# Kernel optimization log

Hardware: AMD Instinct MI355X
Metric: run time of the kernel (lower is better)

Reference implementation:

```python
import jax, jax.numpy as jnp
import numpy as np

NUM_HEADS = 16
NEG_INF = float('-inf')


def setup_inputs() -> dict:
    key = jax.random.key(0)
    ks = jax.random.split(key, 8)
    B, S, D = 2, 2048, 1024
    return {
        "query": jax.random.normal(ks[0], (B, S, D), jnp.float32),
        "key": jax.random.normal(ks[1], (B, S, D), jnp.float32),
        "value": jax.random.normal(ks[2], (B, S, D), jnp.float32),
        "attention_mask": jnp.zeros((B, S, S), dtype=bool),
        "Wq": jax.random.normal(ks[3], (D, D), jnp.float32) * (D ** -0.5),
        "Wk": jax.random.normal(ks[4], (D, D), jnp.float32) * (D ** -0.5),
        "Wv": jax.random.normal(ks[5], (D, D), jnp.float32) * (D ** -0.5),
        "Wout": jax.random.normal(ks[6], (D, D), jnp.float32) * (D ** -0.5),
        "b_out": jnp.zeros((D,), jnp.float32),
        "is_causal": 1,
    }


def reference(query, key, value, attention_mask, Wq, Wk, Wv, Wout, b_out, is_causal):
    B, q_len, D = query.shape
    k_len = key.shape[1]
    H = NUM_HEADS
    dk = D // H
    # projections (torch Linear: x @ W.T), split heads -> [B, H, S, dk]
    q = (query @ Wq.T).reshape(B, q_len, H, dk).transpose(0, 2, 1, 3)
    k = (key @ Wk.T).reshape(B, k_len, H, dk).transpose(0, 2, 1, 3)
    v = (value @ Wv.T).reshape(B, k_len, H, dk).transpose(0, 2, 1, 3)
    scores = jnp.einsum('bhqd,bhkd->bhqk', q, k) / jnp.sqrt(jnp.float32(dk))
    if is_causal:
        causal = jnp.triu(jnp.ones((q_len, k_len), dtype=bool), k=1)
        scores = jnp.where(causal, NEG_INF, scores)
    # attn_mask True -> masked out; broadcast over heads
    scores = jnp.where(attention_mask[:, None, :, :], NEG_INF, scores)
    attn = jax.nn.softmax(scores, axis=-1)
    attn = jnp.where(jnp.isnan(attn), 0.0, attn)  # fully-masked rows -> 0
    out = jnp.einsum('bhqk,bhkd->bhqd', attn, v)
    out = out.transpose(0, 2, 1, 3).reshape(B, q_len, D)
    return out @ Wout.T + b_out
```

## Files before the change

kernel.cpp:

```cpp
#include <hip/hip_runtime.h>
#include <hip/hip_bf16.h>

typedef __attribute__((ext_vector_type(8))) short bf16x8;
typedef __attribute__((ext_vector_type(4))) float f32x4;
typedef unsigned long long u64;
typedef unsigned int u32;

#define MFMA(a,b,c) __builtin_amdgcn_mfma_f32_16x16x32_bf16(a,b,c,0,0,0)
#define NEG_INF (-__builtin_inff())
#define SCALE2 0.1803368801111244f

__device__ __forceinline__ unsigned short f2b(float f) {
  unsigned int u = __float_as_uint(f);
  u = u + 0x7fffu + ((u >> 16) & 1u);
  return (unsigned short)(u >> 16);
}

__device__ __forceinline__ u32 pkbf(float lo, float hi) {
  __hip_bfloat162 h = __float22bfloat162_rn(float2{lo, hi});
  return *reinterpret_cast<u32*>(&h);
}

__device__ __forceinline__ void gload_lds16(const unsigned short* g, unsigned short* l) {
  __builtin_amdgcn_global_load_lds((const __attribute__((address_space(1))) void*)g,
                                   (__attribute__((address_space(3))) void*)l, 16, 0, 0);
}

__global__ void cvt7(const float* s0, const float* s1, const float* s2,
                     const float* s3, const float* s4, const float* s5, const float* s6,
                     unsigned short* d0, unsigned short* d1, unsigned short* d2,
                     unsigned short* d3, unsigned short* d4, unsigned short* d5, unsigned short* d6,
                     int nbig, int nsmall) {
  const float* s; unsigned short* d; int n4;
  switch (blockIdx.y) {
    case 0: s=s0; d=d0; n4=nbig; break;
    case 1: s=s1; d=d1; n4=nbig; break;
    case 2: s=s2; d=d2; n4=nbig; break;
    case 3: s=s3; d=d3; n4=nsmall; break;
    case 4: s=s4; d=d4; n4=nsmall; break;
    case 5: s=s5; d=d5; n4=nsmall; break;
    default: s=s6; d=d6; n4=nsmall; break;
  }
  int i = blockIdx.x * blockDim.x + threadIdx.x;
  if (i < n4) {
    float4 v = reinterpret_cast<const float4*>(s)[i];
    ushort4 o;
    o.x = f2b(v.x); o.y = f2b(v.y); o.z = f2b(v.z); o.w = f2b(v.w);
    reinterpret_cast<ushort4*>(d)[i] = o;
  }
}

__global__ void pack_mask(const unsigned char* __restrict__ am, u64* __restrict__ pm, int nU) {
  int lane = threadIdx.x & 63;
  int wid = blockIdx.x * (blockDim.x >> 6) + (threadIdx.x >> 6);
  int stride = gridDim.x * (blockDim.x >> 6);
  for (int u = wid; u < nU; u += stride) {
    unsigned char v = am[(size_t)u * 64 + lane];
    u64 m = __ballot(v != 0);
    if (lane == 0) pm[u] = m;
  }
}

__global__ void mask_summary(const u64* __restrict__ pm, u32* __restrict__ ms, int rows, int nkt) {
  int lane = threadIdx.x & 63;
  int wid = (blockIdx.x * blockDim.x + threadIdx.x) >> 6;
  int nw = (gridDim.x * blockDim.x) >> 6;
  for (int rp = wid; rp < (rows >> 1); rp += nw) {
    int row = rp * 2 + (lane >> 5);
    int t = lane & 31;
    u64 v = pm[(size_t)row * nkt + t];
    u64 bm = __ballot(v != 0ULL);
    if (lane == 0)  ms[rp*2]     = (u32)bm;
    if (lane == 32) ms[rp*2 + 1] = (u32)(bm >> 32);
  }
}

__global__ __launch_bounds__(256) void qkv128s(
    const unsigned short* __restrict__ A,
    const unsigned short* __restrict__ Bw,
    unsigned short* __restrict__ Cqk,
    unsigned short* __restrict__ Cv)
{
  const int K = 1024;
  __shared__ unsigned short As[128*32];
  __shared__ unsigned short Bs[128*32];
  const int tid  = threadIdx.x;
  const int w    = tid >> 6, lane = tid & 63;
  const int wr   = w >> 1,   wc   = w & 1;
  const int g    = lane >> 4, li  = lane & 15;
  const int m0   = blockIdx.x * 128, n0 = blockIdx.y * 128;
  const int bq0  = (m0 >> 12) * 1024 + n0;

  f32x4 acc[4][4] = {};

  const int rS0 = (w*2+0)*16 + (lane>>2);
  const int rS1 = (w*2+1)*16 + (lane>>2);
  const int cS  = (lane&3)*8;
  const unsigned short* gA0 = A  + (size_t)(m0+rS0)*K + cS;
  const unsigned short* gA1 = A  + (size_t)(m0+rS1)*K + cS;
  const unsigned short* gB0 = Bw + (size_t)(bq0+rS0)*K + cS;
  const unsigned short* gB1 = Bw + (size_t)(bq0+rS1)*K + cS;
  unsigned short* lA0 = &As[(w*2+0)*512];
  unsigned short* lA1 = &As[(w*2+1)*512];
  unsigned short* lB0 = &Bs[(w*2+0)*512];
  unsigned short* lB1 = &Bs[(w*2+1)*512];

  for (int k0 = 0; k0 < K; k0 += 32) {
    gload_lds16(gA0 + k0, lA0);
    gload_lds16(gA1 + k0, lA1);
    gload_lds16(gB0 + k0, lB0);
    gload_lds16(gB1 + k0, lB1);
    __syncthreads();

    bf16x8 af[4], bf[4];
    #pragma unroll
    for (int i = 0; i < 4; ++i)
      af[i] = *(const bf16x8*)(&As[(wr*64 + i*16 + li)*32 + g*8]);
    #pragma unroll
    for (int j = 0; j < 4; ++j)
      bf[j] = *(const bf16x8*)(&Bs[(wc*64 + j*16 + li)*32 + g*8]);
    #pragma unroll
    for (int i = 0; i < 4; ++i)
      #pragma unroll
      for (int j = 0; j < 4; ++j)
        acc[i][j] = MFMA(af[i], bf[j], acc[i][j]);
    __syncthreads();
  }

  #pragma unroll
  for (int i = 0; i < 4; ++i) {
    #pragma unroll
    for (int j = 0; j < 4; ++j) {
      int col = n0 + wc*64 + j*16 + li;
      #pragma unroll
      for (int r = 0; r < 4; ++r) {
        int row = m0 + wr*64 + i*16 + g*4 + r;
        float v = acc[i][j][r];
        if (row < 8192) {
          size_t addr = (((size_t)(row >> 11) * 16 + (col >> 6)) * 2048 + (row & 2047)) * 64 + (col & 63);
          Cqk[addr] = f2b(v);
        } else {
          int tk = row & 4095;
          size_t addr = (((size_t)(tk >> 11) * 16 + (col >> 6)) * 64 + (col & 63)) * 2048 + (tk & 2047);
          Cv[addr] = f2b(v);
        }
      }
    }
  }
}

__global__ __launch_bounds__(256) void gemm64x64(
    const unsigned short* __restrict__ A,
    const unsigned short* __restrict__ Bw,
    float* __restrict__ Cf,
    const float* __restrict__ bias,
    int M, int N, int K)
{
  const int NT = 32;
  __shared__ unsigned short As[2][64*32];
  __shared__ unsigned short Bs[2][64*32];
  const int tid  = threadIdx.x;
  const int w    = tid >> 6, lane = tid & 63;
  const int wr   = w >> 1,   wc   = w & 1;
  const int g    = lane >> 4, li  = lane & 15;
  const int m0   = blockIdx.x * 64, n0 = blockIdx.y * 64;

  f32x4 acc[2][2] = {};
  const int crow = lane >> 2, ccol = (lane & 3) * 8;
  const unsigned short* gA = A  + (size_t)(m0 + w*16 + crow)*K + ccol;
  const unsigned short* gB = Bw + (size_t)(n0 + w*16 + crow)*K + ccol;

  gload_lds16(gA, &As[0][w*512]);
  gload_lds16(gB, &Bs[0][w*512]);
  __syncthreads();

  for (int t = 0; t < NT; ++t) {
    const int cur = t & 1;
    if (t + 1 < NT) {
      const int k1 = (t + 1) * 32;
      gload_lds16(gA + k1, &As[cur^1][w*512]);
      gload_lds16(gB + k1, &Bs[cur^1][w*512]);
    }
    bf16x8 af[2], bf[2];
    #pragma unroll
    for (int i = 0; i < 2; ++i)
      af[i] = *(const bf16x8*)(&As[cur][(wr*32 + i*16 + li)*32 + g*8]);
    #pragma unroll
    for (int j = 0; j < 2; ++j)
      bf[j] = *(const bf16x8*)(&Bs[cur][(wc*32 + j*16 + li)*32 + g*8]);
    #pragma unroll
    for (int i = 0; i < 2; ++i)
      #pragma unroll
      for (int j = 0; j < 2; ++j)
        acc[i][j] = MFMA(af[i], bf[j], acc[i][j]);
    __syncthreads();
  }

  #pragma unroll
  for (int i = 0; i < 2; ++i) {
    #pragma unroll
    for (int j = 0; j < 2; ++j) {
      int col = n0 + wc*32 + j*16 + li;
      #pragma unroll
      for (int r = 0; r < 4; ++r) {
        int row = m0 + wr*32 + i*16 + g*4 + r;
        Cf[(size_t)row*N + col] = acc[i][j][r] + bias[col];
      }
    }
  }
}

__global__ __launch_bounds__(256, 4) void attn_kernel(
    const unsigned short* __restrict__ Qh,
    const unsigned short* __restrict__ Kh,
    const unsigned short* __restrict__ Vt,
    const u64* __restrict__ pmask,
    const u32* __restrict__ msum,
    const int* __restrict__ causal_p,
    unsigned short* __restrict__ Ob,
    int B, int H, int S)
{
  __shared__ unsigned short Ks [64*64];
  __shared__ unsigned short Vts[64*64];

  const int tid = threadIdx.x, w = tid >> 6, lane = tid & 63;
  const int g = lane >> 4, li = lane & 15;
  const int nkt = S >> 6, nqt = S >> 6;
  const int causal = causal_p[0];

  int id = blockIdx.x;
  int par = (id ^ (id >> 8)) & 1;
  int qh  = ((id >> 1) & 15) ^ (((id >> 8) & 3) << 2);
  int bh  = id >> 5;
  int qt  = par ? (nqt - 1 - qh) : qh;
  const int q0 = qt << 6;
  const int b = bh / H, h = bh % H;
  const size_t baseK = (size_t)bh * S * 64;
  const size_t baseV = (size_t)bh * 64 * S;

  const int qg = q0 + w*16 + li;
  const unsigned short* qp = Qh + baseK + (size_t)qg*64 + g*8;
  const bf16x8 qf0 = *(const bf16x8*)(qp);
  const bf16x8 qf1 = *(const bf16x8*)(qp + 32);

  const u32 sOr = msum[(size_t)b*S + qg];

  f32x4 oacc[4] = {};
  float mrun = -1e30f, lrun = 0.f;

  const int colk  = (lane & 7) ^ ((lane >> 3) & 7);
  const int ldrow = lane >> 3;
  const int ntile = causal ? (qt + 1) : nkt;

  for (int t = 0; t < ntile; ++t) {
    const int kv0 = t << 6;
    __syncthreads();
    #pragma unroll
    for (int s2 = 0; s2 < 2; ++s2) {
      int u = w*2 + s2;
      gload_lds16(Kh + baseK + (size_t)(kv0 + u*8 + ldrow)*64 + colk*8, &Ks[u*512]);
      gload_lds16(Vt + baseV + (size_t)(u*8 + ldrow)*S + kv0 + colk*8, &Vts[u*512]);
    }
    __syncthreads();

    f32x4 sa[4];
    #pragma unroll
    for (int ni = 0; ni < 4; ++ni) sa[ni] = (f32x4){0.f, 0.f, 0.f, 0.f};
    #pragma unroll
    for (int ni = 0; ni < 4; ++ni) {
      int row = ni*16 + li, rx = row & 7;
      bf16x8 k0 = *(const bf16x8*)(&Ks[row*64 + ((g     ^ rx))*8]);
      bf16x8 k1 = *(const bf16x8*)(&Ks[row*64 + (((4+g) ^ rx))*8]);
      sa[ni] = MFMA(k0, qf0, sa[ni]);
      sa[ni] = MFMA(k1, qf1, sa[ni]);
    }

    const bool edge   = (causal != 0) && (t == ntile - 1);
    const bool doMask = __any(((sOr >> t) & 1u) != 0u);
    float corr = 1.0f;
    bool rescale = true;

    if (!edge && !doMask) {
      float pe[4][4];
      #pragma unroll
      for (int ni = 0; ni < 4; ++ni)
        #pragma unroll
        for (int r = 0; r < 4; ++r)
          pe[ni][r] = exp2f(fmaf(sa[ni][r], SCALE2, -mrun));
      float a0 = fmaxf(sa[0][0], sa[0][1]), a1 = fmaxf(sa[0][2], sa[0][3]);
      float a2 = fmaxf(sa[1][0], sa[1][1]), a3 = fmaxf(sa[1][2], sa[1][3]);
      float a4 = fmaxf(sa[2][0], sa[2][1]), a5 = fmaxf(sa[2][2], sa[2][3]);
      float a6 = fmaxf(sa[3][0], sa[3][1]), a7 = fmaxf(sa[3][2], sa[3][3]);
      float mx = fmaxf(fmaxf(fmaxf(a0,a1), fmaxf(a2,a3)),
                       fmaxf(fmaxf(a4,a5), fmaxf(a6,a7)));
      mx = fmaxf(mx, __shfl_xor(mx, 16));
      mx = fmaxf(mx, __shfl_xor(mx, 32));
      float mxs = mx * SCALE2;
      if (__all(mxs <= mrun + 8.0f)) {
        float s0 = (pe[0][0]+pe[0][1]) + (pe[0][2]+pe[0][3]);
        float s1 = (pe[1][0]+pe[1][1]) + (pe[1][2]+pe[1][3]);
        float s2 = (pe[2][0]+pe[2][1]) + (pe[2][2]+pe[2][3]);
        float s3 = (pe[3][0]+pe[3][1]) + (pe[3][2]+pe[3][3]);
        float rs = (s0+s1) + (s2+s3);
        rs += __shfl_xor(rs, 16);
        rs += __shfl_xor(rs, 32);
        lrun += rs;
        #pragma unroll
        for (int ni = 0; ni < 4; ++ni)
          #pragma unroll
          for (int r = 0; r < 4; ++r)
            sa[ni][r] = pe[ni][r];
        rescale = false;
      } else {
        float mu = fmaxf(mrun, mxs);
        corr = exp2f(mrun - mu);
        float rs = 0.f;
        #pragma unroll
        for (int ni = 0; ni < 4; ++ni)
          #pragma unroll
          for (int r = 0; r < 4; ++r) {
            float p = exp2f(fmaf(sa[ni][r], SCALE2, -mu));
            sa[ni][r] = p;
            rs += p;
          }
        rs += __shfl_xor(rs, 16);
        rs += __shfl_xor(rs, 32);
        lrun = lrun * corr + rs;
        mrun = mu;
      }
    } else {
      u64 mrow = doMask ? pmask[((size_t)b*S + qg) * nkt + t] : 0ULL;
      #pragma unroll
      for (int ni = 0; ni < 4; ++ni)
        #pragma unroll
        for (int r = 0; r < 4; ++r) {
          int kvloc = ni*16 + g*4 + r;
          bool dead = (edge && (kv0 + kvloc > qg)) || ((mrow >> kvloc) & 1ULL);
          sa[ni][r] = dead ? NEG_INF : sa[ni][r] * SCALE2;
        }
      float mx = sa[0][0];
      #pragma unroll
      for (int ni = 0; ni < 4; ++ni)
        #pragma unroll
        for (int r = 0; r < 4; ++r)
          if (ni + r) mx = fmaxf(mx, sa[ni][r]);
      mx = fmaxf(mx, __shfl_xor(mx, 16));
      mx = fmaxf(mx, __shfl_xor(mx, 32));
      float mu = fmaxf(mrun, mx);
      corr = exp2f(mrun - mu);
      float rs = 0.f;
      #pragma unroll
      for (int ni = 0; ni < 4; ++ni)
        #pragma unroll
        for (int r = 0; r < 4; ++r) {
          float pe = exp2f(sa[ni][r] - mu);
          sa[ni][r] = pe;
          rs += pe;
        }
      rs += __shfl_xor(rs, 16);
      rs += __shfl_xor(rs, 32);
      lrun = lrun * corr + rs;
      mrun = mu;
    }

    bf16x8 pf[2];
    #pragma unroll
    for (int c = 0; c < 2; ++c) {
      u32 PA0 = pkbf(sa[2*c  ][0], sa[2*c  ][1]);
      u32 PA1 = pkbf(sa[2*c  ][2], sa[2*c  ][3]);
      u32 PB0 = pkbf(sa[2*c+1][0], sa[2*c+1][1]);
      u32 PB1 = pkbf(sa[2*c+1][2], sa[2*c+1][3]);
      u32 X16_0 = (u32)__shfl_xor((int)((g==2) ? PB0 : PA0), 16);
      u32 X16_1 = (u32)__shfl_xor((int)((g==2) ? PB1 : PA1), 16);
      u32 X32_0 = (u32)__shfl_xor((int)((g==0) ? PB0 : PA0), 32);
      u32 X32_1 = (u32)__shfl_xor((int)((g==0) ? PB1 : PA1), 32);
      u32 X48_0 = (u32)__shfl_xor((int)((g==1) ? PB0 : PA0), 48);
      u32 X48_1 = (u32)__shfl_xor((int)((g==1) ? PB1 : PA1), 48);
      union { u32 u[4]; bf16x8 v; } pbu;
      pbu.u[0] = (g==0) ? PA0   : (g==1) ? X48_0 : (g==2) ? X32_0 : X16_0;
      pbu.u[1] = (g==0) ? PA1   : (g==1) ? X48_1 : (g==2) ? X32_1 : X16_1;
      pbu.u[2] = (g==0) ? X16_0 : (g==1) ? X32_0 : (g==2) ? X48_0 : PB0;
      pbu.u[3] = (g==0) ? X16_1 : (g==1) ? X32_1 : (g==2) ? X48_1 : PB1;
      pf[c] = pbu.v;
    }

    if (rescale) {
      #pragma unroll
      for (int di = 0; di < 4; ++di) {
        oacc[di][0] *= corr; oacc[di][1] *= corr;
        oacc[di][2] *= corr; oacc[di][3] *= corr;
      }
    }

    #pragma unroll
    for (int c = 0; c < 2; ++c) {
      #pragma unroll
      for (int di = 0; di < 4; ++di) {
        int d = di*16 + li;
        bf16x8 vf = *(const bf16x8*)(&Vts[d*64 + (((c*4+g) ^ (d&7)))*8]);
        oacc[di] = MFMA(vf, pf[c], oacc[di]);
      }
    }
  }

  __syncthreads();
  unsigned short* scr = &Ks[w*1024];
  float rl = (lrun > 0.f) ? 1.0f / lrun : 0.f;
  #pragma unroll
  for (int di = 0; di < 4; ++di)
    #pragma unroll
    for (int r = 0; r < 4; ++r) {
      int d = di*16 + g*4 + r;
      scr[li*64 + (((d>>3) ^ (li&7)))*8 + (d&7)] = f2b(oacc[di][r] * rl);
    }
  const int D = H * 64;
  #pragma unroll
  for (int rr = 0; rr < 2; ++rr) {
    int q = rr*8 + (lane >> 3);
    int sl = lane & 7;
    bf16x8 v = *(const bf16x8*)(&scr[q*64 + ((sl ^ (q & 7)))*8]);
    *(bf16x8*)(Ob + (size_t)(b*S + q0 + w*16 + q)*D + h*64 + sl*8) = v;
  }
}

extern "C" void kernel_launch(void* const* d_in, const int* in_sizes, int n_in,
                              void* d_out, int out_size, void* d_ws, size_t ws_size,
                              hipStream_t stream) {
  const float* query = (const float*)d_in[0];
  const float* key_  = (const float*)d_in[1];
  const float* value = (const float*)d_in[2];
  const unsigned char* amask = (const unsigned char*)d_in[3];
  const float* Wq   = (const float*)d_in[4];
  const float* Wk   = (const float*)d_in[5];
  const float* Wv   = (const float*)d_in[6];
  const float* Wout = (const float*)d_in[7];
  const float* b_out = (const float*)d_in[8];
  const int* is_causal = (const int*)d_in[9];
  float* out = (float*)d_out;

  const int B = 2, S = 2048, D = 1024, H = 16;
  const int M = B * S;
  const size_t nx = (size_t)M * D;
  const size_t nw = (size_t)D * D;
  const int nU = B * S * (S / 64);

  unsigned short* ws = (unsigned short*)d_ws;
  unsigned short* xq = ws;
  unsigned short* xk = xq + nx;
  unsigned short* xv = xk + nx;
  unsigned short* wq = xv + nx;
  unsigned short* wk = wq + nw;
  unsigned short* wv = wk + nw;
  unsigned short* wo = wv + nw;
  unsigned short* qb = wo + nw;
  unsigned short* kb = qb + nx;
  unsigned short* vt = kb + nx;
  u32* msum = (u32*)(vt + nx);
  unsigned short* ob = xq;
  u64* pmask = (u64*)xv;

  cvt7<<<dim3((unsigned)(nx/4/256), 7), 256, 0, stream>>>(
      query, key_, value, Wq, Wk, Wv, Wout,
      xq, xk, xv, wq, wk, wv, wo, (int)(nx/4), (int)(nw/4));

  qkv128s<<<dim3(3*M/128, D/128), 256, 0, stream>>>(xq, wq, qb, vt);

  pack_mask<<<512, 256, 0, stream>>>(amask, pmask, nU);
  mask_summary<<<128, 256, 0, stream>>>(pmask, msum, M, S/64);

  attn_kernel<<<dim3((S/64) * B * H), 256, 0, stream>>>(qb, kb, vt, pmask, msum, is_causal, ob, B, H, S);

  gemm64x64<<<dim3(M/64, D/64), 256, 0, stream>>>(ob, wo, out, b_out, M, D, D);
}
```

Before: 168.0 us.

## Split causal attention KV range across blocks with split-K combine kernel

Replaces the one-block-per-query-tile attention grid with a split-KV scheme. Longer causal query tiles are split into 2-4 segments so per-block work is more even, and the grid grows to 2560 blocks. Partial outputs (bf16), row maxima and sums go to workspace, and a new combine kernel merges them with log-sum-exp weights. This targets tail imbalance from the causal triangle. The cost is an extra launch, extra global traffic for the partials, and bf16 rounding of the unnormalized partial outputs.

```diff
diff --git a/kernel.cpp b/kernel.cpp
--- a/kernel.cpp
+++ b/kernel.cpp
@@ -14,6 +14,11 @@
   unsigned int u = __float_as_uint(f);
   u = u + 0x7fffu + ((u >> 16) & 1u);
   return (unsigned short)(u >> 16);
+}
+
+__device__ __forceinline__ float b2f(unsigned short s) {
+  unsigned int u = ((unsigned int)s) << 16;
+  return __uint_as_float(u);
 }
 
 __device__ __forceinline__ u32 pkbf(float lo, float hi) {
@@ -210,6 +215,151 @@
   }
 }
 
+__device__ __forceinline__ void attn_tile(
+    const unsigned short* __restrict__ Ks, const unsigned short* __restrict__ Vts,
+    const bf16x8& qf0, const bf16x8& qf1,
+    float& mrun, float& lrun, f32x4* oacc,
+    bool edge, bool doMask, const u64* __restrict__ prow,
+    int t, int kv0, int qg, int g, int li)
+{
+  f32x4 sa[4];
+  #pragma unroll
+  for (int ni = 0; ni < 4; ++ni) sa[ni] = (f32x4){0.f, 0.f, 0.f, 0.f};
+  #pragma unroll
+  for (int ni = 0; ni < 4; ++ni) {
+    int row = ni*16 + li, rx = row & 7;
+    bf16x8 k0 = *(const bf16x8*)(&Ks[row*64 + ((g     ^ rx))*8]);
+    bf16x8 k1 = *(const bf16x8*)(&Ks[row*64 + (((4+g) ^ rx))*8]);
+    sa[ni] = MFMA(k0, qf0, sa[ni]);
+    sa[ni] = MFMA(k1, qf1, sa[ni]);
+  }
+
+  float corr = 1.0f;
+  bool rescale = true;
+
+  if (!edge && !doMask) {
+    float pe[4][4];
+    #pragma unroll
+    for (int ni = 0; ni < 4; ++ni)
+      #pragma unroll
+      for (int r = 0; r < 4; ++r)
+        pe[ni][r] = exp2f(fmaf(sa[ni][r], SCALE2, -mrun));
+    float a0 = fmaxf(sa[0][0], sa[0][1]), a1 = fmaxf(sa[0][2], sa[0][3]);
+    float a2 = fmaxf(sa[1][0], sa[1][1]), a3 = fmaxf(sa[1][2], sa[1][3]);
+    float a4 = fmaxf(sa[2][0], sa[2][1]), a5 = fmaxf(sa[2][2], sa[2][3]);
+    float a6 = fmaxf(sa[3][0], sa[3][1]), a7 = fmaxf(sa[3][2], sa[3][3]);
+    float mx = fmaxf(fmaxf(fmaxf(a0,a1), fmaxf(a2,a3)),
+                     fmaxf(fmaxf(a4,a5), fmaxf(a6,a7)));
+    mx = fmaxf(mx, __shfl_xor(mx, 16));
+    mx = fmaxf(mx, __shfl_xor(mx, 32));
+    float mxs = mx * SCALE2;
+    if (__all(mxs <= mrun + 8.0f)) {
+      float s0 = (pe[0][0]+pe[0][1]) + (pe[0][2]+pe[0][3]);
+      float s1 = (pe[1][0]+pe[1][1]) + (pe[1][2]+pe[1][3]);
+      float s2 = (pe[2][0]+pe[2][1]) + (pe[2][2]+pe[2][3]);
+      float s3 = (pe[3][0]+pe[3][1]) + (pe[3][2]+pe[3][3]);
+      float rs = (s0+s1) + (s2+s3);
+      rs += __shfl_xor(rs, 16);
+      rs += __shfl_xor(rs, 32);
+      lrun += rs;
+      #pragma unroll
+      for (int ni = 0; ni < 4; ++ni)
+        #pragma unroll
+        for (int r = 0; r < 4; ++r)
+          sa[ni][r] = pe[ni][r];
+      rescale = false;
+    } else {
+      float mu = fmaxf(mrun, mxs);
+      corr = exp2f(mrun - mu);
+      float rs = 0.f;
+      #pragma unroll
+      for (int ni = 0; ni < 4; ++ni)
+        #pragma unroll
+        for (int r = 0; r < 4; ++r) {
+          float p = exp2f(fmaf(sa[ni][r], SCALE2, -mu));
+          sa[ni][r] = p;
+          rs += p;
+        }
+      rs += __shfl_xor(rs, 16);
+      rs += __shfl_xor(rs, 32);
+      lrun = lrun * corr + rs;
+      mrun = mu;
+    }
+  } else {
+    u64 mrow = doMask ? prow[t] : 0ULL;
+    #pragma unroll
+    for (int ni = 0; ni < 4; ++ni)
+      #pragma unroll
+      for (int r = 0; r < 4; ++r) {
+        int kvloc = ni*16 + g*4 + r;
+        bool dead = (edge && (kv0 + kvloc > qg)) || ((mrow >> kvloc) & 1ULL);
+        sa[ni][r] = dead ? NEG_INF : sa[ni][r] * SCALE2;
+      }
+    float mx = sa[0][0];
+    #pragma unroll
+    for (int ni = 0; ni < 4; ++ni)
+      #pragma unroll
+      for (int r = 0; r < 4; ++r)
+        if (ni + r) mx = fmaxf(mx, sa[ni][r]);
+    mx = fmaxf(mx, __shfl_xor(mx, 16));
+    mx = fmaxf(mx, __shfl_xor(mx, 32));
+    float mu = fmaxf(mrun, mx);
+    corr = exp2f(mrun - mu);
+    float rs = 0.f;
+    #pragma unroll
+    for (int ni = 0; ni < 4; ++ni)
+      #pragma unroll
+      for (int r = 0; r < 4; ++r) {
+        float pe = exp2f(sa[ni][r] - mu);
+        sa[ni][r] = pe;
+        rs += pe;
+      }
+    rs += __shfl_xor(rs, 16);
+    rs += __shfl_xor(rs, 32);
+    lrun = lrun * corr + rs;
+    mrun = mu;
+  }
+
+  bf16x8 pf[2];
+  #pragma unroll
+  for (int c = 0; c < 2; ++c) {
+    u32 PA0 = pkbf(sa[2*c  ][0], sa[2*c  ][1]);
+    u32 PA1 = pkbf(sa[2*c  ][2], sa[2*c  ][3]);
+    u32 PB0 = pkbf(sa[2*c+1][0], sa[2*c+1][1]);
+    u32 PB1 = pkbf(sa[2*c+1][2], sa[2*c+1][3]);
+    u32 X16_0 = (u32)__shfl_xor((int)((g==2) ? PB0 : PA0), 16);
+    u32 X16_1 = (u32)__shfl_xor((int)((g==2) ? PB1 : PA1), 16);
+    u32 X32_0 = (u32)__shfl_xor((int)((g==0) ? PB0 : PA0), 32);
+    u32 X32_1 = (u32)__shfl_xor((int)((g==0) ? PB1 : PA1), 32);
+    u32 X48_0 = (u32)__shfl_xor((int)((g==1) ? PB0 : PA0), 48);
+    u32 X48_1 = (u32)__shfl_xor((int)((g==1) ? PB1 : PA1), 48);
+    union { u32 u[4]; bf16x8 v; } pbu;
+    pbu.u[0] = (g==0) ? PA0   : (g==1) ? X48_0 : (g==2) ? X32_0 : X16_0;
+    pbu.u[1] = (g==0) ? PA1   : (g==1) ? X48_1 : (g==2) ? X32_1 : X16_1;
+    pbu.u[2] = (g==0) ? X16_0 : (g==1) ? X32_0 : (g==2) ? X48_0 : PB0;
+    pbu.u[3] = (g==0) ? X16_1 : (g==1) ? X32_1 : (g==2) ? X48_1 : PB1;
+    pf[c] = pbu.v;
+  }
+
+  if (rescale) {
+    #pragma unroll
+    for (int di = 0; di < 4; ++di) {
+      oacc[di][0] *= corr; oacc[di][1] *= corr;
+      oacc[di][2] *= corr; oacc[di][3] *= corr;
+    }
+  }
+
+  #pragma unroll
+  for (int c = 0; c < 2; ++c) {
+    #pragma unroll
+    for (int di = 0; di < 4; ++di) {
+      int d = di*16 + li;
+      bf16x8 vf = *(const bf16x8*)(&Vts[d*64 + (((c*4+g) ^ (d&7)))*8]);
+      oacc[di] = MFMA(vf, pf[c], oacc[di]);
+    }
+  }
+}
+
 __global__ __launch_bounds__(256, 4) void attn_kernel(
     const unsigned short* __restrict__ Qh,
     const unsigned short* __restrict__ Kh,
@@ -218,6 +368,9 @@
     const u32* __restrict__ msum,
     const int* __restrict__ causal_p,
     unsigned short* __restrict__ Ob,
+    unsigned short* __restrict__ Opart,
+    float* __restrict__ Mp,
+    float* __restrict__ Lp,
     int B, int H, int S)
 {
   __shared__ unsigned short Ks [64*64];
@@ -225,34 +378,47 @@
 
   const int tid = threadIdx.x, w = tid >> 6, lane = tid & 63;
   const int g = lane >> 4, li = lane & 15;
-  const int nkt = S >> 6, nqt = S >> 6;
+  const int nkt = S >> 6;
   const int causal = causal_p[0];
-
-  int id = blockIdx.x;
-  int par = (id ^ (id >> 8)) & 1;
-  int qh  = ((id >> 1) & 15) ^ (((id >> 8) & 3) << 2);
-  int bh  = id >> 5;
-  int qt  = par ? (nqt - 1 - qh) : qh;
-  const int q0 = qt << 6;
-  const int b = bh / H, h = bh % H;
+  const int j = blockIdx.x;
+
+  int bh, qt, seg, k, t0, t1;
+  if (causal) {
+    bh = j / 80;
+    int jj = 79 - (j - bh*80);
+    if (jj < 8)       { qt = jj;              seg = 0;      k = 1; }
+    else if (jj < 24) { int x = jj-8;  qt = 8  + (x>>1); seg = x&1;      k = 2; }
+    else if (jj < 48) { int x = jj-24; int q3 = x/3; qt = 16 + q3; seg = x - q3*3; k = 3; }
+    else              { int x = jj-48; qt = 24 + (x>>2); seg = x&3;      k = 4; }
+    int nt = qt + 1;
+    t0 = (seg*nt)/k; t1 = ((seg+1)*nt)/k;
+  } else {
+    if (j >= 2048) return;
+    bh = j >> 6;
+    int jj = j & 63;
+    qt = jj >> 1; seg = jj & 1; k = 2;
+    t0 = seg*16; t1 = t0 + 16;
+  }
+
+  const int b = bh >> 4, h = bh & 15;
   const size_t baseK = (size_t)bh * S * 64;
   const size_t baseV = (size_t)bh * 64 * S;
-
+  const int colk  = (lane & 7) ^ ((lane >> 3) & 7);
+  const int ldrow = lane >> 3;
+  const int D = H * 64;
+
+  const int q0 = qt << 6;
   const int qg = q0 + w*16 + li;
   const unsigned short* qp = Qh + baseK + (size_t)qg*64 + g*8;
   const bf16x8 qf0 = *(const bf16x8*)(qp);
   const bf16x8 qf1 = *(const bf16x8*)(qp + 32);
-
   const u32 sOr = msum[(size_t)b*S + qg];
+  const u64* prow = pmask + (size_t)(b*S + qg) * nkt;
 
   f32x4 oacc[4] = {};
   float mrun = -1e30f, lrun = 0.f;
 
-  const int colk  = (lane & 7) ^ ((lane >> 3) & 7);
-  const int ldrow = lane >> 3;
-  const int ntile = causal ? (qt + 1) : nkt;
-
-  for (int t = 0; t < ntile; ++t) {
+  for (int t = t0; t < t1; ++t) {
     const int kv0 = t << 6;
     __syncthreads();
     #pragma unroll
@@ -262,165 +428,107 @@
       gload_lds16(Vt + baseV + (size_t)(u*8 + ldrow)*S + kv0 + colk*8, &Vts[u*512]);
     }
     __syncthreads();
-
-    f32x4 sa[4];
-    #pragma unroll
-    for (int ni = 0; ni < 4; ++ni) sa[ni] = (f32x4){0.f, 0.f, 0.f, 0.f};
-    #pragma unroll
-    for (int ni = 0; ni < 4; ++ni) {
-      int row = ni*16 + li, rx = row & 7;
-      bf16x8 k0 = *(const bf16x8*)(&Ks[row*64 + ((g     ^ rx))*8]);
-      bf16x8 k1 = *(const bf16x8*)(&Ks[row*64 + (((4+g) ^ rx))*8]);
-      sa[ni] = MFMA(k0, qf0, sa[ni]);
-      sa[ni] = MFMA(k1, qf1, sa[ni]);
-    }
-
-    const bool edge   = (causal != 0) && (t == ntile - 1);
+    const bool edge = (causal != 0) && (t == qt);
     const bool doMask = __any(((sOr >> t) & 1u) != 0u);
-    float corr = 1.0f;
-    bool rescale = true;
-
-    if (!edge && !doMask) {
-      float pe[4][4];
-      #pragma unroll
-      for (int ni = 0; ni < 4; ++ni)
-        #pragma unroll
-        for (int r = 0; r < 4; ++r)
-          pe[ni][r] = exp2f(fmaf(sa[ni][r], SCALE2, -mrun));
-      float a0 = fmaxf(sa[0][0], sa[0][1]), a1 = fmaxf(sa[0][2], sa[0][3]);
-      float a2 = fmaxf(sa[1][0], sa[1][1]), a3 = fmaxf(sa[1][2], sa[1][3]);
-      float a4 = fmaxf(sa[2][0], sa[2][1]), a5 = fmaxf(sa[2][2], sa[2][3]);
-      float a6 = fmaxf(sa[3][0], sa[3][1]), a7 = fmaxf(sa[3][2], sa[3][3]);
-      float mx = fmaxf(fmaxf(fmaxf(a0,a1), fmaxf(a2,a3)),
-                       fmaxf(fmaxf(a4,a5), fmaxf(a6,a7)));
-      mx = fmaxf(mx, __shfl_xor(mx, 16));
-      mx = fmaxf(mx, __shfl_xor(mx, 32));
-      float mxs = mx * SCALE2;
-      if (__all(mxs <= mrun + 8.0f)) {
-        float s0 = (pe[0][0]+pe[0][1]) + (pe[0][2]+pe[0][3]);
-        float s1 = (pe[1][0]+pe[1][1]) + (pe[1][2]+pe[1][3]);
-        float s2 = (pe[2][0]+pe[2][1]) + (pe[2][2]+pe[2][3]);
-        float s3 = (pe[3][0]+pe[3][1]) + (pe[3][2]+pe[3][3]);
-        float rs = (s0+s1) + (s2+s3);
-        rs += __shfl_xor(rs, 16);
-        rs += __shfl_xor(rs, 32);
-        lrun += rs;
-        #pragma unroll
-        for (int ni = 0; ni < 4; ++ni)
-          #pragma unroll
-          for (int r = 0; r < 4; ++r)
-            sa[ni][r] = pe[ni][r];
-        rescale = false;
-      } else {
-        float mu = fmaxf(mrun, mxs);
-        corr = exp2f(mrun - mu);
-        float rs = 0.f;
-        #pragma unroll
-        for (int ni = 0; ni < 4; ++ni)
-          #pragma unroll
-          for (int r = 0; r < 4; ++r) {
-            float p = exp2f(fmaf(sa[ni][r], SCALE2, -mu));
-            sa[ni][r] = p;
-            rs += p;
-          }
-        rs += __shfl_xor(rs, 16);
-        rs += __shfl_xor(rs, 32);
-        lrun = lrun * corr + rs;
-        mrun = mu;
+    attn_tile(Ks, Vts, qf0, qf1, mrun, lrun, oacc, edge, doMask, prow, t, kv0, qg, g, li);
+  }
+
+  if (k == 1) {
+    __syncthreads();
+    unsigned short* scr = &Ks[w*1024];
+    float rl = (lrun > 0.f) ? 1.0f / lrun : 0.f;
+    #pragma unroll
+    for (int di = 0; di < 4; ++di)
+      #pragma unroll
+      for (int r = 0; r < 4; ++r) {
+        int d = di*16 + g*4 + r;
+        scr[li*64 + (((d>>3) ^ (li&7)))*8 + (d&7)] = f2b(oacc[di][r] * rl);
       }
+    #pragma unroll
+    for (int rr = 0; rr < 2; ++rr) {
+      int q = rr*8 + (lane >> 3);
+      int sl = lane & 7;
+      bf16x8 v = *(const bf16x8*)(&scr[q*64 + ((sl ^ (q & 7)))*8]);
+      *(bf16x8*)(Ob + (size_t)(b*S + q0 + w*16 + q)*D + h*64 + sl*8) = v;
+    }
+  } else {
+    int local;
+    if (causal) {
+      local = (qt < 16) ? (2*(qt-8) + seg)
+            : (qt < 24) ? (16 + 3*(qt-16) + seg)
+                        : (40 + 4*(qt-24) + seg);
     } else {
-      u64 mrow = doMask ? pmask[((size_t)b*S + qg) * nkt + t] : 0ULL;
-      #pragma unroll
-      for (int ni = 0; ni < 4; ++ni)
-        #pragma unroll
-        for (int r = 0; r < 4; ++r) {
-          int kvloc = ni*16 + g*4 + r;
-          bool dead = (edge && (kv0 + kvloc > qg)) || ((mrow >> kvloc) & 1ULL);
-          sa[ni][r] = dead ? NEG_INF : sa[ni][r] * SCALE2;
-        }
-      float mx = sa[0][0];
-      #pragma unroll
-      for (int ni = 0; ni < 4; ++ni)
-        #pragma unroll
-        for (int r = 0; r < 4; ++r)
-          if (ni + r) mx = fmaxf(mx, sa[ni][r]);
-      mx = fmaxf(mx, __shfl_xor(mx, 16));
-      mx = fmaxf(mx, __shfl_xor(mx, 32));
-      float mu = fmaxf(mrun, mx);
-      corr = exp2f(mrun - mu);
-      float rs = 0.f;
-      #pragma unroll
-      for (int ni = 0; ni < 4; ++ni)
-        #pragma unroll
-        for (int r = 0; r < 4; ++r) {
-          float pe = exp2f(sa[ni][r] - mu);
-          sa[ni][r] = pe;
-          rs += pe;
-        }
-      rs += __shfl_xor(rs, 16);
-      rs += __shfl_xor(rs, 32);
-      lrun = lrun * corr + rs;
-      mrun = mu;
-    }
-
-    bf16x8 pf[2];
-    #pragma unroll
-    for (int c = 0; c < 2; ++c) {
-      u32 PA0 = pkbf(sa[2*c  ][0], sa[2*c  ][1]);
-      u32 PA1 = pkbf(sa[2*c  ][2], sa[2*c  ][3]);
-      u32 PB0 = pkbf(sa[2*c+1][0], sa[2*c+1][1]);
-      u32 PB1 = pkbf(sa[2*c+1][2], sa[2*c+1][3]);
-      u32 X16_0 = (u32)__shfl_xor((int)((g==2) ? PB0 : PA0), 16);
-      u32 X16_1 = (u32)__shfl_xor((int)((g==2) ? PB1 : PA1), 16);
-      u32 X32_0 = (u32)__shfl_xor((int)((g==0) ? PB0 : PA0), 32);
-      u32 X32_1 = (u32)__shfl_xor((int)((g==0) ? PB1 : PA1), 32);
-      u32 X48_0 = (u32)__shfl_xor((int)((g==1) ? PB0 : PA0), 48);
-      u32 X48_1 = (u32)__shfl_xor((int)((g==1) ? PB1 : PA1), 48);
-      union { u32 u[4]; bf16x8 v; } pbu;
-      pbu.u[0] = (g==0) ? PA0   : (g==1) ? X48_0 : (g==2) ? X32_0 : X16_0;
-      pbu.u[1] = (g==0) ? PA1   : (g==1) ? X48_1 : (g==2) ? X32_1 : X16_1;
-      pbu.u[2] = (g==0) ? X16_0 : (g==1) ? X32_0 : (g==2) ? X48_0 : PB0;
-      pbu.u[3] = (g==0) ? X16_1 : (g==1) ? X32_1 : (g==2) ? X48_1 : PB1;
-      pf[c] = pbu.v;
-    }
-
-    if (rescale) {
-      #pragma unroll
-      for (int di = 0; di < 4; ++di) {
-        oacc[di][0] *= corr; oacc[di][1] *= corr;
-        oacc[di][2] *= corr; oacc[di][3] *= corr;
-      }
-    }
-
-    #pragma unroll
-    for (int c = 0; c < 2; ++c) {
-      #pragma unroll
-      for (int di = 0; di < 4; ++di) {
-        int d = di*16 + li;
-        bf16x8 vf = *(const bf16x8*)(&Vts[d*64 + (((c*4+g) ^ (d&7)))*8]);
-        oacc[di] = MFMA(vf, pf[c], oacc[di]);
-      }
-    }
-  }
-
-  __syncthreads();
-  unsigned short* scr = &Ks[w*1024];
-  float rl = (lrun > 0.f) ? 1.0f / lrun : 0.f;
-  #pragma unroll
-  for (int di = 0; di < 4; ++di)
-    #pragma unroll
-    for (int r = 0; r < 4; ++r) {
-      int d = di*16 + g*4 + r;
-      scr[li*64 + (((d>>3) ^ (li&7)))*8 + (d&7)] = f2b(oacc[di][r] * rl);
-    }
+      local = qt*2 + seg;
+    }
+    const int rec = bh*72 + local;
+    unsigned short* dst = Opart + (size_t)rec*4096 + (w*64 + lane)*16;
+    #pragma unroll
+    for (int di = 0; di < 4; ++di)
+      #pragma unroll
+      for (int r = 0; r < 4; ++r)
+        dst[di*4 + r] = f2b(oacc[di][r]);
+    if (g == 0) { Mp[rec*64 + w*16 + li] = mrun; Lp[rec*64 + w*16 + li] = lrun; }
+  }
+}
+
+__global__ __launch_bounds__(256) void attn_combine(
+    const unsigned short* __restrict__ Opart,
+    const float* __restrict__ Mp, const float* __restrict__ Lp,
+    const int* __restrict__ causal_p,
+    unsigned short* __restrict__ Ob, int H, int S)
+{
+  const int causal = causal_p[0];
+  const int blk = blockIdx.x;
+  int bh, qt, k, local0;
+  if (causal) {
+    if (blk >= 768) return;
+    bh = blk / 24;
+    int qq = blk - bh*24;
+    qt = 8 + qq;
+    if (qt < 16)      { k = 2; local0 = 2*(qt-8); }
+    else if (qt < 24) { k = 3; local0 = 16 + 3*(qt-16); }
+    else              { k = 4; local0 = 40 + 4*(qt-24); }
+  } else {
+    bh = blk >> 5; qt = blk & 31; k = 2; local0 = qt*2;
+  }
+  const int recb = bh*72 + local0;
+  const int b = bh >> 4, h = bh & 15;
+  const int tid = threadIdx.x;
+  const int q = tid >> 2;
+  const int dbase = (tid & 3) * 16;
+  const int w = q >> 4, li = q & 15;
   const int D = H * 64;
-  #pragma unroll
-  for (int rr = 0; rr < 2; ++rr) {
-    int q = rr*8 + (lane >> 3);
-    int sl = lane & 7;
-    bf16x8 v = *(const bf16x8*)(&scr[q*64 + ((sl ^ (q & 7)))*8]);
-    *(bf16x8*)(Ob + (size_t)(b*S + q0 + w*16 + q)*D + h*64 + sl*8) = v;
-  }
+
+  float ms[4], ls[4];
+  float m = -1e30f;
+  for (int s = 0; s < k; ++s) {
+    ms[s] = Mp[(recb+s)*64 + q];
+    ls[s] = Lp[(recb+s)*64 + q];
+    m = fmaxf(m, ms[s]);
+  }
+  float wgt[4];
+  float denom = 0.f;
+  for (int s = 0; s < k; ++s) {
+    wgt[s] = exp2f(ms[s] - m);
+    denom += wgt[s] * ls[s];
+  }
+  float rden = (denom > 0.f) ? 1.0f/denom : 0.f;
+  for (int s = 0; s < k; ++s) wgt[s] *= rden;
+
+  unsigned short outv[16];
+  #pragma unroll
+  for (int kk = 0; kk < 16; ++kk) {
+    int d = dbase + kk;
+    int di = d >> 4, g2 = (d >> 2) & 3, r = d & 3;
+    int idx = (w*64 + g2*16 + li)*16 + di*4 + r;
+    float o = 0.f;
+    for (int s = 0; s < k; ++s)
+      o += wgt[s] * b2f(Opart[(size_t)(recb+s)*4096 + idx]);
+    outv[kk] = f2b(o);
+  }
+  unsigned short* dst = Ob + (size_t)(b*S + qt*64 + q)*D + h*64 + dbase;
+  #pragma unroll
+  for (int kk = 0; kk < 16; ++kk) dst[kk] = outv[kk];
 }
 
 extern "C" void kernel_launch(void* const* d_in, const int* in_sizes, int n_in,
@@ -456,8 +564,11 @@
   unsigned short* kb = qb + nx;
   unsigned short* vt = kb + nx;
   u32* msum = (u32*)(vt + nx);
+  u64* pmask = (u64*)(msum + 16384);
   unsigned short* ob = xq;
-  u64* pmask = (u64*)xv;
+  unsigned short* Opart = xk;
+  float* Mp = (float*)wk;
+  float* Lp = Mp + 2304*64;
 
   cvt7<<<dim3((unsigned)(nx/4/256), 7), 256, 0, stream>>>(
       query, key_, value, Wq, Wk, Wv, Wout,
@@ -468,7 +579,9 @@
   pack_mask<<<512, 256, 0, stream>>>(amask, pmask, nU);
   mask_summary<<<128, 256, 0, stream>>>(pmask, msum, M, S/64);
 
-  attn_kernel<<<dim3((S/64) * B * H), 256, 0, stream>>>(qb, kb, vt, pmask, msum, is_causal, ob, B, H, S);
+  attn_kernel<<<dim3(2560), 256, 0, stream>>>(qb, kb, vt, pmask, msum, is_causal,
+                                              ob, Opart, Mp, Lp, B, H, S);
+  attn_combine<<<dim3(1024), 256, 0, stream>>>(Opart, Mp, Lp, is_causal, ob, H, S);
 
   gemm64x64<<<dim3(M/64, D/64), 256, 0, stream>>>(ob, wo, out, b_out, M, D, D);
 }
```

Result: slower. 180.7 us (+7.5%).
